# Performance work log

Measured on AMD Instinct MI355X. Metric: run time of the kernel, lower is better.

The kernel has to match this reference:

```python
import jax, jax.numpy as jnp
import numpy as np

EPS = 1e-5

def _act_quant(x):
    # per-token absmax int8 quantization (BitNet b1.58)
    scale = 127.0 / jnp.clip(jnp.max(jnp.abs(x), axis=-1, keepdims=True), EPS)
    return jnp.clip(jnp.round(x * scale), -128.0, 127.0) / scale

def _weight_quant(w):
    # per-tensor absmean ternary quantization {-1, 0, +1}
    scale = 1.0 / jnp.clip(jnp.mean(jnp.abs(w)), EPS)
    return jnp.clip(jnp.round(w * scale), -1.0, 1.0) / scale

def _bitlinear(x, w):
    # STE: forward uses quantized values, gradient passes through
    xq = x + jax.lax.stop_gradient(_act_quant(x) - x)
    wq = w + jax.lax.stop_gradient(_weight_quant(w) - w)
    # torch Linear: y = x @ W.T, W is [out, in]
    return jnp.einsum('bsd,od->bso', xq, wq)

def setup_inputs() -> dict:
    key = jax.random.key(0)
    k1, k2, k3, k4 = jax.random.split(key, 4)
    B, S, D = 8, 2048, 512
    x = jax.random.normal(k1, (B, S, D), dtype=jnp.float32)
    s = (1.0 / D) ** 0.5
    Wq = jax.random.normal(k2, (D, D), dtype=jnp.float32) * s
    Wk = jax.random.normal(k3, (D, D), dtype=jnp.float32) * s
    Wv = jax.random.normal(k4, (D, D), dtype=jnp.float32) * s
    return {"x": x, "Wq": Wq, "Wk": Wk, "Wv": Wv}

def reference(x, Wq, Wk, Wv):
    B, S, D = x.shape
    q = _bitlinear(x, Wq)
    k = _bitlinear(x, Wk)
    v = _bitlinear(x, Wv)
    # NOTE: original scales by batch_size**-0.5 (faithful to source)
    scores = jnp.einsum('bqd,bkd->bqk', q, k) * (B ** -0.5)
    causal = jnp.tril(jnp.ones((S, S), dtype=bool))  # tril[:S, :S]
    scores = jnp.where(causal, scores, -jnp.inf)
    attn = jax.nn.softmax(scores, axis=-1)
    return jnp.einsum('bqk,bkd->bqd', attn, v)
```

## Files before the change

kernel.cpp:

```cpp
#include <hip/hip_runtime.h>
#include <cstdint>
#include <cstddef>

#define BATCH 8
#define SEQ   2048
#define DDIM  512
#define NROW  (BATCH*SEQ)
#define KPACK (DDIM/4)
#define EPSQ  1e-5f
#define FSCALE 0.35355339059327373f

typedef _Float16 half8 __attribute__((ext_vector_type(8)));
typedef _Float16 half4 __attribute__((ext_vector_type(4)));
typedef float    f32x4 __attribute__((ext_vector_type(4)));
typedef int      i32x4 __attribute__((ext_vector_type(4)));

static constexpr size_t OFF_M   = 0;
static constexpr size_t OFF_WP  = 256;
static constexpr size_t OFF_XQ  = OFF_WP + (size_t)3*KPACK*DDIM*4;
static constexpr size_t OFF_SX  = OFF_XQ + (size_t)NROW*KPACK*4;
static constexpr size_t OFF_QKV = OFF_SX + (size_t)NROW*4;
static constexpr size_t OFF_PO  = OFF_QKV + (size_t)3*NROW*DDIM*2;
static constexpr size_t OFF_PM  = OFF_PO + (size_t)512*64*512*4;
static constexpr size_t OFF_PL  = OFF_PM + (size_t)512*64*4;

__device__ __forceinline__ int q8(float v, float s) {
  int i = (int)rintf(v * s);
  i = i < -128 ? -128 : (i > 127 ? 127 : i);
  return i & 0xff;
}

__device__ __forceinline__ void gld_lds16(const _Float16* g, _Float16* l) {
  __builtin_amdgcn_global_load_lds(
      (const __attribute__((address_space(1))) void*)g,
      (__attribute__((address_space(3))) void*)l, 16, 0, 0);
}

__global__ __launch_bounds__(256) void wsum_kernel(
    const float* __restrict__ Wq, const float* __restrict__ Wk,
    const float* __restrict__ Wv, float* __restrict__ mw) {
  const float* W = blockIdx.y == 0 ? Wq : (blockIdx.y == 1 ? Wk : Wv);
  __shared__ float red[256];
  const float4* p = (const float4*)(W + blockIdx.x * 8192);
  float s = 0.f;
  #pragma unroll
  for (int i = 0; i < 8; i++) {
    float4 a = p[i * 256 + threadIdx.x];
    s += fabsf(a.x) + fabsf(a.y) + fabsf(a.z) + fabsf(a.w);
  }
  red[threadIdx.x] = s;
  __syncthreads();
  for (int w = 128; w > 0; w >>= 1) {
    if ((int)threadIdx.x < w) red[threadIdx.x] += red[threadIdx.x + w];
    __syncthreads();
  }
  if (threadIdx.x == 0) atomicAdd(&mw[blockIdx.y], red[0]);
}

__global__ __launch_bounds__(256) void wquant_kernel(
    const float* __restrict__ Wq, const float* __restrict__ Wk,
    const float* __restrict__ Wv, const float* __restrict__ mw,
    int* __restrict__ wp) {
  int idx = blockIdx.x * 256 + threadIdx.x;
  int mat = idx >> 16;
  int local = idx & 0xFFFF;
  int o  = local >> 7;
  int k4 = local & 127;
  const float* W = mat == 0 ? Wq : (mat == 1 ? Wk : Wv);
  float mean = mw[mat] * (1.0f / 262144.0f);
  float scale = 1.0f / fmaxf(mean, EPSQ);
  float4 w4 = *(const float4*)(W + (size_t)o * DDIM + k4 * 4);
  int t0 = (int)rintf(w4.x * scale); t0 = t0 < -1 ? -1 : (t0 > 1 ? 1 : t0);
  int t1 = (int)rintf(w4.y * scale); t1 = t1 < -1 ? -1 : (t1 > 1 ? 1 : t1);
  int t2 = (int)rintf(w4.z * scale); t2 = t2 < -1 ? -1 : (t2 > 1 ? 1 : t2);
  int t3 = (int)rintf(w4.w * scale); t3 = t3 < -1 ? -1 : (t3 > 1 ? 1 : t3);
  int packed = (t0 & 0xff) | ((t1 & 0xff) << 8) | ((t2 & 0xff) << 16) | ((t3 & 0xff) << 24);
  wp[((size_t)mat * DDIM + o) * KPACK + k4] = packed;
}

__global__ __launch_bounds__(256) void aquant_kernel(
    const float* __restrict__ x, int* __restrict__ xq, float* __restrict__ sx) {
  int wid = threadIdx.x >> 6, lane = threadIdx.x & 63;
  int row = blockIdx.x * 4 + wid;
  const float* xr = x + (size_t)row * DDIM;
  float4 a = ((const float4*)xr)[lane];
  float4 b = ((const float4*)xr)[64 + lane];
  float amax = fmaxf(fmaxf(fmaxf(fabsf(a.x), fabsf(a.y)), fmaxf(fabsf(a.z), fabsf(a.w))),
                     fmaxf(fmaxf(fabsf(b.x), fabsf(b.y)), fmaxf(fabsf(b.z), fabsf(b.w))));
  for (int off = 32; off > 0; off >>= 1) amax = fmaxf(amax, __shfl_xor(amax, off, 64));
  float aa = fmaxf(amax, EPSQ);
  float scale = 127.0f / aa;
  int p0 = q8(a.x, scale) | (q8(a.y, scale) << 8) | (q8(a.z, scale) << 16) | (q8(a.w, scale) << 24);
  int p1 = q8(b.x, scale) | (q8(b.y, scale) << 8) | (q8(b.z, scale) << 16) | (q8(b.w, scale) << 24);
  xq[(size_t)row * KPACK + lane]      = p0;
  xq[(size_t)row * KPACK + 64 + lane] = p1;
  if (lane == 0) sx[row] = aa * (1.0f / 127.0f);
}

__global__ __launch_bounds__(256, 2) void qkv_gemm_kernel(
    const int* __restrict__ xq, const int* __restrict__ wp,
    const float* __restrict__ sx, const float* __restrict__ mw,
    _Float16* __restrict__ qkv) {
  __shared__ __align__(16) int xs[64][132];
  __shared__ __align__(16) int bs[64][132];
  __shared__ float sxs[64];

  const int tid  = threadIdx.x;
  const int w    = tid >> 6;
  const int lane = tid & 63;
  const int quad = lane >> 4;
  const int col  = lane & 15;

  const int r0g = blockIdx.x * 64;
  const int n0  = blockIdx.y * 64;
  const int mat = blockIdx.z;

  {
    const i32x4* src = (const i32x4*)(xq + (size_t)r0g * KPACK);
    #pragma unroll
    for (int i = 0; i < 8; i++) {
      int e = i * 256 + tid;
      int row = e >> 5, u = e & 31;
      *(i32x4*)&xs[row][u * 4] = src[e];
    }
  }
  {
    const i32x4* src = (const i32x4*)(wp + ((size_t)mat * DDIM + n0) * KPACK);
    #pragma unroll
    for (int i = 0; i < 8; i++) {
      int e = i * 256 + tid;
      int c = e >> 5, u = e & 31;
      *(i32x4*)&bs[c][u * 4] = src[e];
    }
  }
  if (tid < 64) sxs[tid] = sx[r0g + tid];
  __syncthreads();

  i32x4 acc[4];
  #pragma unroll
  for (int rt = 0; rt < 4; rt++) acc[rt] = (i32x4)(0);

  #pragma unroll
  for (int s = 0; s < 8; s++) {
    i32x4 bf = *(const i32x4*)&bs[w * 16 + col][s * 16 + quad * 4];
    #pragma unroll
    for (int rt = 0; rt < 4; rt++) {
      i32x4 af = *(const i32x4*)&xs[rt * 16 + col][s * 16 + quad * 4];
      acc[rt] = __builtin_amdgcn_mfma_i32_16x16x64_i8(af, bf, acc[rt], 0, 0, 0);
    }
  }

  const float mval = fmaxf(mw[mat] * (1.0f / 262144.0f), EPSQ);
  const int nw = n0 + w * 16 + col;

  if (mat < 2) {
    _Float16* outb = qkv + (size_t)mat * NROW * DDIM;
    #pragma unroll
    for (int rt = 0; rt < 4; rt++) {
      #pragma unroll
      for (int reg = 0; reg < 4; reg++) {
        int rowl = rt * 16 + quad * 4 + reg;
        outb[(size_t)(r0g + rowl) * DDIM + nw] =
            (_Float16)((float)acc[rt][reg] * sxs[rowl] * mval);
      }
    }
  } else {
    _Float16* vT = qkv + (size_t)2 * NROW * DDIM;
    #pragma unroll
    for (int rt = 0; rt < 4; rt++) {
      half4 hv;
      #pragma unroll
      for (int reg = 0; reg < 4; reg++) {
        int rowl = rt * 16 + quad * 4 + reg;
        hv[reg] = (_Float16)((float)acc[rt][reg] * sxs[rowl] * mval);
      }
      int r = r0g + rt * 16 + quad * 4;
      int b = r >> 11, kt = (r & 2047) >> 5, kin = r & 31;
      *(half4*)(vT + ((((size_t)b * 64 + kt) * 512 + nw) * 32 + kin)) = hv;
    }
  }
}

__global__ __launch_bounds__(512, 2) void flash_kernel(
    const _Float16* __restrict__ q, const _Float16* __restrict__ k,
    const _Float16* __restrict__ vT, _Float16* __restrict__ po,
    float* __restrict__ pm, float* __restrict__ pl) {
  __shared__ __align__(16) _Float16 Ksh[2][32][520];
  __shared__ __align__(16) _Float16 VtL[2][512][32];
  __shared__ __align__(16) float    PsS[64 * 33];
  __shared__ __align__(16) _Float16 Pf[64 * 40];
  __shared__ float alpha_l[64];

  const int tid  = threadIdx.x;
  const int w    = tid >> 6;
  const int lane = tid & 63;
  const int quad = lane >> 4;
  const int col  = lane & 15;
  const int rt   = w & 3;
  const int kh   = w >> 2;
  const int smrow = tid >> 3;
  const int sme   = tid & 7;
  const int d0  = w * 64;

  const int vrl = lane >> 2;
  const int vu  = lane & 3;

  const int bb = blockIdx.x & 7;
  const int qi = blockIdx.x >> 3;

  for (int ph = 0; ph < 2; ph++) {
    const int qt = ph ? (31 - qi) : qi;
    const int h  = ph;
    const int slot = ((qt * 8 + bb) * 2 + h);
    const int nT = qt + 1;

    const int qrow0 = qt * 64;
    const size_t bbase = (size_t)bb * SEQ * DDIM;
    const _Float16* kb_p = k + bbase;
    const _Float16* vt_p = vT + (size_t)bb * 64 * 512 * 32;

    half8 qfrag[16];
    {
      const _Float16* qrow_p = q + bbase + (size_t)(qrow0 + rt * 16 + col) * DDIM;
      #pragma unroll
      for (int s = 0; s < 16; s++)
        qfrag[s] = *(const half8*)(qrow_p + s * 32 + quad * 8);
    }

    float m_run = -INFINITY, l_run = 0.f;
    f32x4 o[4][4];
    #pragma unroll
    for (int a = 0; a < 4; a++)
      #pragma unroll
      for (int b2 = 0; b2 < 4; b2++) o[a][b2] = (f32x4)(0.f);

    #pragma unroll
    for (int i = 0; i < 4; i++)
      gld_lds16(kb_p + (size_t)(h * 32 + w * 4 + i) * DDIM + lane * 8,
                &Ksh[0][w * 4 + i][0]);
    {
      const _Float16* vtile = vt_p + (size_t)h * 512 * 32;
      #pragma unroll
      for (int i = 0; i < 4; i++) {
        int r = w * 64 + i * 16 + vrl;
        int su = vu ^ ((r >> 1) & 3);
        gld_lds16(vtile + (size_t)r * 32 + su * 8, &VtL[0][w * 64 + i * 16][0]);
      }
    }
    __syncthreads();

    for (int t = 0; t < nT; t++) {
      const int cur = t & 1, nxt = cur ^ 1;
      const int kb0 = (2 * t + h) * 32;

      if (t + 1 < nT) {
        const int kb1 = kb0 + 64;
        #pragma unroll
        for (int i = 0; i < 4; i++)
          gld_lds16(kb_p + (size_t)(kb1 + w * 4 + i) * DDIM + lane * 8,
                    &Ksh[nxt][w * 4 + i][0]);
        const _Float16* vtile = vt_p + (size_t)(2 * t + h + 2) * 512 * 32;
        #pragma unroll
        for (int i = 0; i < 4; i++) {
          int r = w * 64 + i * 16 + vrl;
          int su = vu ^ ((r >> 1) & 3);
          gld_lds16(vtile + (size_t)r * 32 + su * 8, &VtL[nxt][w * 64 + i * 16][0]);
        }
      }

      {
        f32x4 c = (f32x4)(0.f);
        #pragma unroll
        for (int s = 0; s < 16; s++) {
          half8 b = *(const half8*)&Ksh[cur][kh * 16 + col][s * 32 + quad * 8];
          c = __builtin_amdgcn_mfma_f32_16x16x32_f16(qfrag[s], b, c, 0, 0, 0);
        }
        #pragma unroll
        for (int reg = 0; reg < 4; reg++)
          PsS[(rt * 16 + quad * 4 + reg) * 33 + kh * 16 + col] = c[reg];
      }
      __syncthreads();

      {
        const int qrow = qrow0 + smrow;
        float sv[4];
        #pragma unroll
        for (int i = 0; i < 4; i++) {
          float s = PsS[smrow * 33 + sme * 4 + i] * FSCALE;
          if (kb0 + sme * 4 + i > qrow) s = -INFINITY;
          sv[i] = s;
        }
        float mx = fmaxf(fmaxf(sv[0], sv[1]), fmaxf(sv[2], sv[3]));
        #pragma unroll
        for (int m = 1; m <= 4; m <<= 1) mx = fmaxf(mx, __shfl_xor(mx, m, 64));
        float mn = fmaxf(m_run, mx);
        float mnc = fmaxf(mn, -1e30f);
        float al = __expf(m_run - mnc);
        half4 p4;
        float rs = 0.f;
        #pragma unroll
        for (int i = 0; i < 4; i++) {
          float p = __expf(sv[i] - mnc);
          rs += p;
          p4[i] = (_Float16)p;
        }
        #pragma unroll
        for (int m = 1; m <= 4; m <<= 1) rs += __shfl_xor(rs, m, 64);
        l_run = l_run * al + rs;
        m_run = mn;
        *(half4*)&Pf[smrow * 40 + sme * 4] = p4;
        if (sme == 0) alpha_l[smrow] = al;
      }
      __syncthreads();

      {
        half8 ap[4];
        f32x4 af[4];
        #pragma unroll
        for (int r2 = 0; r2 < 4; r2++) {
          ap[r2] = *(const half8*)&Pf[(r2 * 16 + col) * 40 + quad * 8];
          af[r2] = *(const f32x4*)&alpha_l[r2 * 16 + quad * 4];
        }
        #pragma unroll
        for (int r2 = 0; r2 < 4; r2++)
          #pragma unroll
          for (int ct = 0; ct < 4; ct++)
            o[r2][ct] *= af[r2];
        #pragma unroll
        for (int ct = 0; ct < 4; ct++) {
          int R = d0 + ct * 16 + col;
          int ur = quad ^ ((R >> 1) & 3);
          half8 bv = *(const half8*)&VtL[cur][R][ur * 8];
          #pragma unroll
          for (int r2 = 0; r2 < 4; r2++)
            o[r2][ct] = __builtin_amdgcn_mfma_f32_16x16x32_f16(ap[r2], bv, o[r2][ct], 0, 0, 0);
        }
      }
      __syncthreads();
    }

    if (sme == 0) {
      pm[slot * 64 + smrow] = m_run;
      pl[slot * 64 + smrow] = l_run;
    }
    {
      _Float16* pob = po + (size_t)slot * 64 * 512;
      #pragma unroll
      for (int r2 = 0; r2 < 4; r2++) {
        #pragma unroll
        for (int ct = 0; ct < 4; ct++) {
          #pragma unroll
          for (int e = 0; e < 4; e++) {
            __builtin_nontemporal_store(
                (_Float16)o[r2][ct][e],
                &pob[(size_t)(r2 * 16 + quad * 4 + e) * 512 + d0 + ct * 16 + col]);
          }
        }
      }
    }
  }
}

__global__ __launch_bounds__(256) void merge_kernel(
    const _Float16* __restrict__ po, const float* __restrict__ pm,
    const float* __restrict__ pl, float* __restrict__ out) {
  __shared__ float w0s[64], w1s[64], dns[64];
  const int tid = threadIdx.x;
  const int qt = blockIdx.x, b = blockIdx.y;
  const int slot0 = (qt * 8 + b) * 2;
  const int slot1 = slot0 + 1;

  if (tid < 64) {
    float m0 = pm[slot0 * 64 + tid], m1 = pm[slot1 * 64 + tid];
    float l0 = pl[slot0 * 64 + tid], l1 = pl[slot1 * 64 + tid];
    float ms = fmaxf(m0, m1);
    float a0 = __expf(m0 - ms);
    float a1 = __expf(m1 - ms);
    w0s[tid] = a0;
    w1s[tid] = a1;
    dns[tid] = 1.0f / (a0 * l0 + a1 * l1);
  }
  __syncthreads();

  const half8* p0 = (const half8*)(po + (size_t)slot0 * 64 * 512);
  const half8* p1 = (const half8*)(po + (size_t)slot1 * 64 * 512);
  f32x4* op = (f32x4*)(out + ((size_t)b * SEQ + qt * 64) * 512);
  #pragma unroll 4
  for (int j = 0; j < 16; j++) {
    int e = j * 256 + tid;
    int row = e >> 6;
    half8 a = __builtin_nontemporal_load(p0 + e);
    half8 c = __builtin_nontemporal_load(p1 + e);
    float w0 = w0s[row], w1 = w1s[row], dn = dns[row];
    f32x4 r0, r1;
    #pragma unroll
    for (int u = 0; u < 4; u++) r0[u] = ((float)a[u] * w0 + (float)c[u] * w1) * dn;
    #pragma unroll
    for (int u = 0; u < 4; u++) r1[u] = ((float)a[4 + u] * w0 + (float)c[4 + u] * w1) * dn;
    op[e * 2]     = r0;
    op[e * 2 + 1] = r1;
  }
}

extern "C" void kernel_launch(void* const* d_in, const int* in_sizes, int n_in,
                              void* d_out, int out_size, void* d_ws, size_t ws_size,
                              hipStream_t stream) {
  const float* x  = (const float*)d_in[0];
  const float* Wq = (const float*)d_in[1];
  const float* Wk = (const float*)d_in[2];
  const float* Wv = (const float*)d_in[3];
  float* out = (float*)d_out;
  char* ws = (char*)d_ws;

  float* mw  = (float*)(ws + OFF_M);
  int*   wp  = (int*)(ws + OFF_WP);
  int*   xq  = (int*)(ws + OFF_XQ);
  float* sx  = (float*)(ws + OFF_SX);
  _Float16* qkv = (_Float16*)(ws + OFF_QKV);
  _Float16* qf  = qkv;
  _Float16* kf  = qkv + (size_t)NROW * DDIM;
  _Float16* vTf = qkv + 2 * (size_t)NROW * DDIM;
  _Float16* po = (_Float16*)(ws + OFF_PO);
  float* pm = (float*)(ws + OFF_PM);
  float* pl = (float*)(ws + OFF_PL);

  hipMemsetAsync(mw, 0, 16, stream);
  wsum_kernel<<<dim3(32, 3), 256, 0, stream>>>(Wq, Wk, Wv, mw);
  wquant_kernel<<<768, 256, 0, stream>>>(Wq, Wk, Wv, mw, wp);
  aquant_kernel<<<4096, 256, 0, stream>>>(x, xq, sx);
  qkv_gemm_kernel<<<dim3(256, 8, 3), 256, 0, stream>>>(xq, wp, sx, mw, qkv);
  flash_kernel<<<dim3(256), 512, 0, stream>>>(qf, kf, vTf, po, pm, pl);
  merge_kernel<<<dim3(32, 8), 256, 0, stream>>>(po, pm, pl, out);
}
```

Before: 226.5 us.

## Split flash work into one tile per block and drop LDS double buffering

The flash kernel no longer loops over two phases per block. It launches 512 blocks, each handling one (query tile, half) pair, and removes the double-buffered K/V shared-memory staging so LDS use roughly halves and launch bounds allow 4 blocks per CU. The aim is more concurrent waves to hide load latency through occupancy instead of software prefetch. In exchange, each iteration now waits on its own global-to-LDS load with no overlap, and the paired load balancing within a block is lost, leaving it to the scheduler.

```diff
diff --git a/kernel.cpp b/kernel.cpp
--- a/kernel.cpp
+++ b/kernel.cpp
@@ -181,12 +181,12 @@
   }
 }
 
-__global__ __launch_bounds__(512, 2) void flash_kernel(
+__global__ __launch_bounds__(512, 4) void flash_kernel(
     const _Float16* __restrict__ q, const _Float16* __restrict__ k,
     const _Float16* __restrict__ vT, _Float16* __restrict__ po,
     float* __restrict__ pm, float* __restrict__ pl) {
-  __shared__ __align__(16) _Float16 Ksh[2][32][520];
-  __shared__ __align__(16) _Float16 VtL[2][512][32];
+  __shared__ __align__(16) _Float16 Ksh[32][520];
+  __shared__ __align__(16) _Float16 VtL[512][32];
   __shared__ __align__(16) float    PsS[64 * 33];
   __shared__ __align__(16) _Float16 Pf[64 * 40];
   __shared__ float alpha_l[64];
@@ -206,155 +206,137 @@
   const int vu  = lane & 3;
 
   const int bb = blockIdx.x & 7;
-  const int qi = blockIdx.x >> 3;
-
-  for (int ph = 0; ph < 2; ph++) {
-    const int qt = ph ? (31 - qi) : qi;
-    const int h  = ph;
-    const int slot = ((qt * 8 + bb) * 2 + h);
-    const int nT = qt + 1;
-
-    const int qrow0 = qt * 64;
-    const size_t bbase = (size_t)bb * SEQ * DDIM;
-    const _Float16* kb_p = k + bbase;
-    const _Float16* vt_p = vT + (size_t)bb * 64 * 512 * 32;
-
-    half8 qfrag[16];
+  const int r  = blockIdx.x >> 3;
+  const int h  = r < 32 ? 0 : 1;
+  const int qt = r < 32 ? r : 63 - r;
+  const int nT = qt + 1;
+  const int slot = (qt * 8 + bb) * 2 + h;
+
+  const int qrow0 = qt * 64;
+  const size_t bbase = (size_t)bb * SEQ * DDIM;
+  const _Float16* kb_p = k + bbase;
+  const _Float16* vt_p = vT + (size_t)bb * 64 * 512 * 32;
+
+  half8 qfrag[16];
+  {
+    const _Float16* qrow_p = q + bbase + (size_t)(qrow0 + rt * 16 + col) * DDIM;
+    #pragma unroll
+    for (int s = 0; s < 16; s++)
+      qfrag[s] = *(const half8*)(qrow_p + s * 32 + quad * 8);
+  }
+
+  float m_run = -INFINITY, l_run = 0.f;
+  f32x4 o[4][4];
+  #pragma unroll
+  for (int a = 0; a < 4; a++)
+    #pragma unroll
+    for (int b2 = 0; b2 < 4; b2++) o[a][b2] = (f32x4)(0.f);
+
+  for (int t = 0; t < nT; t++) {
+    const int kt  = 2 * t + h;
+    const int kb0 = kt * 32;
+
+    #pragma unroll
+    for (int i = 0; i < 4; i++)
+      gld_lds16(kb_p + (size_t)(kb0 + w * 4 + i) * DDIM + lane * 8,
+                &Ksh[w * 4 + i][0]);
     {
-      const _Float16* qrow_p = q + bbase + (size_t)(qrow0 + rt * 16 + col) * DDIM;
-      #pragma unroll
-      for (int s = 0; s < 16; s++)
-        qfrag[s] = *(const half8*)(qrow_p + s * 32 + quad * 8);
-    }
-
-    float m_run = -INFINITY, l_run = 0.f;
-    f32x4 o[4][4];
-    #pragma unroll
-    for (int a = 0; a < 4; a++)
-      #pragma unroll
-      for (int b2 = 0; b2 < 4; b2++) o[a][b2] = (f32x4)(0.f);
-
-    #pragma unroll
-    for (int i = 0; i < 4; i++)
-      gld_lds16(kb_p + (size_t)(h * 32 + w * 4 + i) * DDIM + lane * 8,
-                &Ksh[0][w * 4 + i][0]);
+      const _Float16* vtile = vt_p + (size_t)kt * 512 * 32;
+      #pragma unroll
+      for (int i = 0; i < 4; i++) {
+        int rr = w * 64 + i * 16 + vrl;
+        int su = vu ^ ((rr >> 1) & 3);
+        gld_lds16(vtile + (size_t)rr * 32 + su * 8, &VtL[w * 64 + i * 16][0]);
+      }
+    }
+    __syncthreads();
+
     {
-      const _Float16* vtile = vt_p + (size_t)h * 512 * 32;
+      f32x4 c = (f32x4)(0.f);
+      #pragma unroll
+      for (int s = 0; s < 16; s++) {
+        half8 b = *(const half8*)&Ksh[kh * 16 + col][s * 32 + quad * 8];
+        c = __builtin_amdgcn_mfma_f32_16x16x32_f16(qfrag[s], b, c, 0, 0, 0);
+      }
+      #pragma unroll
+      for (int reg = 0; reg < 4; reg++)
+        PsS[(rt * 16 + quad * 4 + reg) * 33 + kh * 16 + col] = c[reg];
+    }
+    __syncthreads();
+
+    {
+      const int qrow = qrow0 + smrow;
+      float sv[4];
       #pragma unroll
       for (int i = 0; i < 4; i++) {
-        int r = w * 64 + i * 16 + vrl;
-        int su = vu ^ ((r >> 1) & 3);
-        gld_lds16(vtile + (size_t)r * 32 + su * 8, &VtL[0][w * 64 + i * 16][0]);
-      }
+        float s = PsS[smrow * 33 + sme * 4 + i] * FSCALE;
+        if (kb0 + sme * 4 + i > qrow) s = -INFINITY;
+        sv[i] = s;
+      }
+      float mx = fmaxf(fmaxf(sv[0], sv[1]), fmaxf(sv[2], sv[3]));
+      #pragma unroll
+      for (int m = 1; m <= 4; m <<= 1) mx = fmaxf(mx, __shfl_xor(mx, m, 64));
+      float mn = fmaxf(m_run, mx);
+      float mnc = fmaxf(mn, -1e30f);
+      float al = __expf(m_run - mnc);
+      half4 p4;
+      float rs = 0.f;
+      #pragma unroll
+      for (int i = 0; i < 4; i++) {
+        float p = __expf(sv[i] - mnc);
+        rs += p;
+        p4[i] = (_Float16)p;
+      }
+      #pragma unroll
+      for (int m = 1; m <= 4; m <<= 1) rs += __shfl_xor(rs, m, 64);
+      l_run = l_run * al + rs;
+      m_run = mn;
+      *(half4*)&Pf[smrow * 40 + sme * 4] = p4;
+      if (sme == 0) alpha_l[smrow] = al;
     }
     __syncthreads();
 
-    for (int t = 0; t < nT; t++) {
-      const int cur = t & 1, nxt = cur ^ 1;
-      const int kb0 = (2 * t + h) * 32;
-
-      if (t + 1 < nT) {
-        const int kb1 = kb0 + 64;
+    {
+      half8 ap[4];
+      f32x4 af[4];
+      #pragma unroll
+      for (int r2 = 0; r2 < 4; r2++) {
+        ap[r2] = *(const half8*)&Pf[(r2 * 16 + col) * 40 + quad * 8];
+        af[r2] = *(const f32x4*)&alpha_l[r2 * 16 + quad * 4];
+      }
+      #pragma unroll
+      for (int r2 = 0; r2 < 4; r2++)
         #pragma unroll
-        for (int i = 0; i < 4; i++)
-          gld_lds16(kb_p + (size_t)(kb1 + w * 4 + i) * DDIM + lane * 8,
-                    &Ksh[nxt][w * 4 + i][0]);
-        const _Float16* vtile = vt_p + (size_t)(2 * t + h + 2) * 512 * 32;
-        #pragma unroll
-        for (int i = 0; i < 4; i++) {
-          int r = w * 64 + i * 16 + vrl;
-          int su = vu ^ ((r >> 1) & 3);
-          gld_lds16(vtile + (size_t)r * 32 + su * 8, &VtL[nxt][w * 64 + i * 16][0]);
-        }
-      }
-
-      {
-        f32x4 c = (f32x4)(0.f);
-        #pragma unroll
-        for (int s = 0; s < 16; s++) {
-          half8 b = *(const half8*)&Ksh[cur][kh * 16 + col][s * 32 + quad * 8];
-          c = __builtin_amdgcn_mfma_f32_16x16x32_f16(qfrag[s], b, c, 0, 0, 0);
-        }
-        #pragma unroll
-        for (int reg = 0; reg < 4; reg++)
-          PsS[(rt * 16 + quad * 4 + reg) * 33 + kh * 16 + col] = c[reg];
-      }
-      __syncthreads();
-
-      {
-        const int qrow = qrow0 + smrow;
-        float sv[4];
-        #pragma unroll
-        for (int i = 0; i < 4; i++) {
-          float s = PsS[smrow * 33 + sme * 4 + i] * FSCALE;
-          if (kb0 + sme * 4 + i > qrow) s = -INFINITY;
-          sv[i] = s;
-        }
-        float mx = fmaxf(fmaxf(sv[0], sv[1]), fmaxf(sv[2], sv[3]));
-        #pragma unroll
-        for (int m = 1; m <= 4; m <<= 1) mx = fmaxf(mx, __shfl_xor(mx, m, 64));
-        float mn = fmaxf(m_run, mx);
-        float mnc = fmaxf(mn, -1e30f);
-        float al = __expf(m_run - mnc);
-        half4 p4;
-        float rs = 0.f;
-        #pragma unroll
-        for (int i = 0; i < 4; i++) {
-          float p = __expf(sv[i] - mnc);
-          rs += p;
-          p4[i] = (_Float16)p;
-        }
-        #pragma unroll
-        for (int m = 1; m <= 4; m <<= 1) rs += __shfl_xor(rs, m, 64);
-        l_run = l_run * al + rs;
-        m_run = mn;
-        *(half4*)&Pf[smrow * 40 + sme * 4] = p4;
-        if (sme == 0) alpha_l[smrow] = al;
-      }
-      __syncthreads();
-
-      {
-        half8 ap[4];
-        f32x4 af[4];
-        #pragma unroll
-        for (int r2 = 0; r2 < 4; r2++) {
-          ap[r2] = *(const half8*)&Pf[(r2 * 16 + col) * 40 + quad * 8];
-          af[r2] = *(const f32x4*)&alpha_l[r2 * 16 + quad * 4];
-        }
+        for (int ct = 0; ct < 4; ct++)
+          o[r2][ct] *= af[r2];
+      #pragma unroll
+      for (int ct = 0; ct < 4; ct++) {
+        int R = d0 + ct * 16 + col;
+        int ur = quad ^ ((R >> 1) & 3);
+        half8 bv = *(const half8*)&VtL[R][ur * 8];
         #pragma unroll
         for (int r2 = 0; r2 < 4; r2++)
-          #pragma unroll
-          for (int ct = 0; ct < 4; ct++)
-            o[r2][ct] *= af[r2];
+          o[r2][ct] = __builtin_amdgcn_mfma_f32_16x16x32_f16(ap[r2], bv, o[r2][ct], 0, 0, 0);
+      }
+    }
+    __syncthreads();
+  }
+
+  if (sme == 0) {
+    pm[slot * 64 + smrow] = m_run;
+    pl[slot * 64 + smrow] = l_run;
+  }
+  {
+    _Float16* pob = po + (size_t)slot * 64 * 512;
+    #pragma unroll
+    for (int r2 = 0; r2 < 4; r2++) {
+      #pragma unroll
+      for (int ct = 0; ct < 4; ct++) {
         #pragma unroll
-        for (int ct = 0; ct < 4; ct++) {
-          int R = d0 + ct * 16 + col;
-          int ur = quad ^ ((R >> 1) & 3);
-          half8 bv = *(const half8*)&VtL[cur][R][ur * 8];
-          #pragma unroll
-          for (int r2 = 0; r2 < 4; r2++)
-            o[r2][ct] = __builtin_amdgcn_mfma_f32_16x16x32_f16(ap[r2], bv, o[r2][ct], 0, 0, 0);
-        }
-      }
-      __syncthreads();
-    }
-
-    if (sme == 0) {
-      pm[slot * 64 + smrow] = m_run;
-      pl[slot * 64 + smrow] = l_run;
-    }
-    {
-      _Float16* pob = po + (size_t)slot * 64 * 512;
-      #pragma unroll
-      for (int r2 = 0; r2 < 4; r2++) {
-        #pragma unroll
-        for (int ct = 0; ct < 4; ct++) {
-          #pragma unroll
-          for (int e = 0; e < 4; e++) {
-            __builtin_nontemporal_store(
-                (_Float16)o[r2][ct][e],
-                &pob[(size_t)(r2 * 16 + quad * 4 + e) * 512 + d0 + ct * 16 + col]);
-          }
+        for (int e = 0; e < 4; e++) {
+          __builtin_nontemporal_store(
+              (_Float16)o[r2][ct][e],
+              &pob[(size_t)(r2 * 16 + quad * 4 + e) * 512 + d0 + ct * 16 + col]);
         }
       }
     }
@@ -429,6 +411,6 @@
   wquant_kernel<<<768, 256, 0, stream>>>(Wq, Wk, Wv, mw, wp);
   aquant_kernel<<<4096, 256, 0, stream>>>(x, xq, sx);
   qkv_gemm_kernel<<<dim3(256, 8, 3), 256, 0, stream>>>(xq, wp, sx, mw, qkv);
-  flash_kernel<<<dim3(256), 512, 0, stream>>>(qf, kf, vTf, po, pm, pl);
+  flash_kernel<<<dim3(512), 512, 0, stream>>>(qf, kf, vTf, po, pm, pl);
   merge_kernel<<<dim3(32, 8), 256, 0, stream>>>(po, pm, pl, out);
 }
```

Result: slower. 394.9 us (+74.4%).
